# Kernel tuning notes

Measured on AMD Instinct MI355X. Metric: run time of the kernel, lower is better.

The kernel has to match this reference:

```python
import jax, jax.numpy as jnp
import numpy as np

B, T, C = 4, 2048, 1024
H, D = 16, 64  # num_heads, head_size


def setup_inputs() -> dict:
    key = jax.random.key(0)
    ks = jax.random.split(key, 5)
    s = 0.02
    x = jax.random.normal(ks[0], (B, T, C), dtype=jnp.float32)
    Wq = jax.random.normal(ks[1], (H, C, D), dtype=jnp.float32) * s
    Wk = jax.random.normal(ks[2], (H, C, D), dtype=jnp.float32) * s
    Wv = jax.random.normal(ks[3], (H, C, D), dtype=jnp.float32) * s
    Wp = jax.random.normal(ks[4], (C, H * D), dtype=jnp.float32) * s  # Linear(H*D, C) weight
    bp = jnp.zeros((C,), dtype=jnp.float32)
    return {"x": x, "Wq": Wq, "Wk": Wk, "Wv": Wv, "Wp": Wp, "bp": bp}


def reference(x, Wq, Wk, Wv, Wp, bp):
    # per-head projections (all heads batched): [B,T,C] x [H,C,D] -> [B,H,T,D]
    q = jnp.einsum('btc,hcd->bhtd', x, Wq)
    k = jnp.einsum('btc,hcd->bhtd', x, Wk)
    v = jnp.einsum('btc,hcd->bhtd', x, Wv)
    scale = 1.0 / jnp.sqrt(jnp.asarray(D, dtype=x.dtype))
    scores = jnp.einsum('bhtd,bhsd->bhts', q, k) * scale  # [B,H,T,T]
    causal = jnp.tril(jnp.ones((T, T), dtype=bool))
    scores = jnp.where(causal, scores, -jnp.inf)
    w = jax.nn.softmax(scores, axis=-1)
    out = jnp.einsum('bhts,bhsd->bhtd', w, v)  # [B,H,T,D]
    out = out.transpose(0, 2, 1, 3).reshape(B, T, H * D)  # concat heads
    return out @ Wp.T + bp  # projection (dropout is identity in eval)
```

## Files before the change

### kernel.cpp

```cpp
#include <hip/hip_runtime.h>
#include <stdint.h>


typedef unsigned short u16;
typedef __attribute__((ext_vector_type(8))) short    s16x8;
typedef __attribute__((ext_vector_type(4))) float    f32x4;
typedef __attribute__((ext_vector_type(2))) uint32_t u32x2;


__device__ __forceinline__ u16 f2b(float f) {
  union { float f; uint32_t u; } v; v.f = f;
  uint32_t r = v.u + 0x7FFFu + ((v.u >> 16) & 1u);
  return (u16)(r >> 16);
}

__device__ __forceinline__ uint32_t cvtpk(float a, float b) {
  uint32_t r;
  asm("v_cvt_pk_bf16_f32 %0, %1, %2" : "=v"(r) : "v"(a), "v"(b));
  return r;
}

__device__ __forceinline__ f32x4 mfma_bf16(s16x8 a, s16x8 b, f32x4 c) {
  asm("v_mfma_f32_16x16x32_bf16 %0, %1, %2, %0" : "+v"(c) : "v"(a), "v"(b));
  return c;
}

__device__ __forceinline__ void gload_lds16(const void* g, void* l) {
  __builtin_amdgcn_global_load_lds(
      (__attribute__((address_space(1))) void*)(uintptr_t)g,
      (__attribute__((address_space(3))) void*)(uint32_t)(uintptr_t)l,
      16, 0, 0);
}


__global__ void cvt_all_kernel(const float* __restrict__ x, const float* __restrict__ Wq,
                               const float* __restrict__ Wk, const float* __restrict__ Wv,
                               const float* __restrict__ Wp, u16* __restrict__ xb,
                               u16* __restrict__ wqkvb, u16* __restrict__ wpb) {
  int bid = blockIdx.x;
  if (bid < 4608) {
    const float* src = (bid < 4096) ? x : Wp;
    u16* dst = (bid < 4096) ? xb : wpb;
    size_t i = (size_t)((bid < 4096) ? bid : (bid - 4096)) * 256 + threadIdx.x;
    const f32x4* pp = (const f32x4*)(src + i * 8);
    f32x4 a = pp[0], b2 = pp[1];
    s16x8 o;
    o[0]=(short)f2b(a[0]); o[1]=(short)f2b(a[1]); o[2]=(short)f2b(a[2]); o[3]=(short)f2b(a[3]);
    o[4]=(short)f2b(b2[0]); o[5]=(short)f2b(b2[1]); o[6]=(short)f2b(b2[2]); o[7]=(short)f2b(b2[3]);
    *(s16x8*)(dst + i * 8) = o;
  } else {
    int idx = (bid - 4608) * 256 + threadIdx.x;
    int sel = idx >> 20;
    int rem = idx & 1048575;
    int n = rem >> 10, c = rem & 1023;
    int h = n >> 6, d = n & 63;
    const float* W = (sel == 0) ? Wq : ((sel == 1) ? Wk : Wv);
    wqkvb[idx] = f2b(W[h * 65536 + c * 64 + d]);
  }
}


template <int MODE>
__global__ __launch_bounds__(256) void gemm_bt_kernel(
    const u16* __restrict__ A, const u16* __restrict__ B, void* __restrict__ Cout,
    const float* __restrict__ bias, u16* __restrict__ vTout, int K, int ldc)
{
  __shared__ __attribute__((aligned(16))) u16 As[128 * 64];
  __shared__ __attribute__((aligned(16))) u16 Bs[128 * 64];

  const int tid  = threadIdx.x;
  const int lane = tid & 63;
  const int w    = tid >> 6;
  const int wm   = w >> 1, wn = w & 1;
  const int g    = lane >> 4;
  const int li   = lane & 15;

  const int nbx = gridDim.x;
  const int nb  = nbx * gridDim.y;
  const int bid = blockIdx.x + nbx * blockIdx.y;
  const int chunk = nb >> 3;
  const int bid2 = (bid & 7) * chunk + (bid >> 3);
  const size_t bm = (size_t)(bid2 % nbx) * 128;
  const size_t bn = (size_t)(bid2 / nbx) * 128;

  f32x4 acc[4][4] = {};

  const int kIters = K >> 6;
  for (int kt = 0; kt < kIters; ++kt) {
    const int kb = kt * 64;
#pragma unroll
    for (int i = 0; i < 4; ++i) {
      int c = i * 256 + tid;
      int row = c >> 3, sl = c & 7;
      int ss = sl ^ (row & 7);
      gload_lds16(A + (bm + row) * K + kb + ss * 8, &As[c * 8]);
      gload_lds16(B + (bn + row) * K + kb + ss * 8, &Bs[c * 8]);
    }
    __syncthreads();
#pragma unroll
    for (int ks = 0; ks < 2; ++ks) {
      s16x8 af[4], bfr[4];
#pragma unroll
      for (int f = 0; f < 4; ++f) {
        int ra = wm * 64 + f * 16 + li;
        int sa = (ks * 4 + g) ^ (ra & 7);
        af[f] = *(const s16x8*)&As[ra * 64 + sa * 8];
        int rb = wn * 64 + f * 16 + li;
        int sb = (ks * 4 + g) ^ (rb & 7);
        bfr[f] = *(const s16x8*)&Bs[rb * 64 + sb * 8];
      }
#pragma unroll
      for (int mi = 0; mi < 4; ++mi)
#pragma unroll
        for (int ni = 0; ni < 4; ++ni)
          acc[mi][ni] = mfma_bf16(af[mi], bfr[ni], acc[mi][ni]);
    }
    __syncthreads();
  }

  if constexpr (MODE == 1) {
#pragma unroll
    for (int ni = 0; ni < 4; ++ni) {
      size_t col = bn + wn * 64 + ni * 16 + li;
      float bv = bias[col];
#pragma unroll
      for (int mi = 0; mi < 4; ++mi)
#pragma unroll
        for (int r = 0; r < 4; ++r) {
          size_t row = bm + wm * 64 + mi * 16 + g * 4 + r;
          ((float*)Cout)[row * ldc + col] = acc[mi][ni][r] + bv;
        }
    }
  } else {
    if (bn < 2048) {
#pragma unroll
      for (int ni = 0; ni < 4; ++ni) {
        size_t col = bn + wn * 64 + ni * 16 + li;
#pragma unroll
        for (int mi = 0; mi < 4; ++mi)
#pragma unroll
          for (int r = 0; r < 4; ++r) {
            size_t row = bm + wm * 64 + mi * 16 + g * 4 + r;
            ((u16*)Cout)[row * ldc + col] = f2b(acc[mi][ni][r]);
          }
      }
    } else {
      const int hb = (int)((bn - 2048) >> 6) + wn;
      const int bb = (int)(bm >> 11);
      const int t0b = ((int)bm & 2047) + wm * 64 + g * 4;
      u16* vrow = vTout + (size_t)((bb * 16 + hb) * 64) * 2048;
#pragma unroll
      for (int ni = 0; ni < 4; ++ni) {
        u16* vd_ = vrow + (size_t)(ni * 16 + li) * 2048;
#pragma unroll
        for (int mi = 0; mi < 4; ++mi) {
          u32x2 wv = { cvtpk(acc[mi][ni][0], acc[mi][ni][1]),
                       cvtpk(acc[mi][ni][2], acc[mi][ni][3]) };
          *(u32x2*)&vd_[t0b + mi * 16] = wv;
        }
      }
    }
  }
}


__global__ __launch_bounds__(256, 4) void attn_kernel(const u16* __restrict__ qkv,
                                                      const u16* __restrict__ vT,
                                                      u16* __restrict__ out) {
  __shared__ __attribute__((aligned(16))) u16 Ks[2][64 * 64];
  __shared__ __attribute__((aligned(16))) u16 Vs[2][64 * 64];
  __shared__ __attribute__((aligned(16))) u16 Ps[4][16 * 64];

  const int id  = blockIdx.x;
  const int xcd = id & 7;
  const int rr  = id >> 3;
  const int bh  = xcd * 8 + (rr & 7);
  const int p   = rr >> 3;

  const int b = bh >> 4, h = bh & 15;
  const int tid = threadIdx.x;
  const int lane = tid & 63;
  const int w = tid >> 6;
  const int g = lane >> 4, li = lane & 15;

  const int tA = 31 - p;
  const int nA = tA + 1;
  const int nTot = 33;

  const u16* kbase = qkv + (size_t)(b * 2048) * 3072 + 1024 + h * 64;
  const u16* vtb   = vT + (size_t)bh * 64 * 2048;
  u16* pl = Ps[w];

  const int srow = tid >> 3;
  const int ssl0 = (tid & 7) ^ (srow & 7);
  const int kge0 = srow * 3072 + ssl0 * 8;
  const int vge0 = srow * 2048 + ssl0 * 8;
  u16* const kd0 = &Ks[0][tid * 8];
  u16* const vd0 = &Vs[0][tid * 8];

  int foff[2][4];
#pragma unroll
  for (int kk = 0; kk < 2; ++kk)
#pragma unroll
    for (int fj = 0; fj < 4; ++fj) {
      int rk = fj * 16 + li;
      foff[kk][fj] = rk * 64 + (((kk * 4 + g) ^ (rk & 7)) * 8);
    }
  const int lsw = li & 14;
  int pwoff[4], proff[2];
#pragma unroll
  for (int fj = 0; fj < 4; ++fj) pwoff[fj] = li * 64 + (((4 * fj + g) ^ lsw) * 4);
#pragma unroll
  for (int kk = 0; kk < 2; ++kk) proff[kk] = li * 64 + (((8 * kk + 2 * g) ^ lsw) * 4);

  auto stage = [&](int buf, int j0) {
    const u16* kp = kbase + (size_t)j0 * 3072;
    const u16* vp = vtb + j0;
    u16* kd = kd0 + buf * 4096;
    u16* vd = vd0 + buf * 4096;
    gload_lds16(kp + kge0, kd);
    gload_lds16(kp + kge0 + 32 * 3072, kd + 2048);
    gload_lds16(vp + vge0, vd);
    gload_lds16(vp + vge0 + 32 * 2048, vd + 2048);
  };

  stage(0, 0);
  __syncthreads();

  s16x8 qf[2];
  f32x4 oacc[4];
  float mrow = -1e30f, lrowp = 0.f;
  int qglob = 0;
  const float cexp = 0.18033688011112042f;
  const float thr = 8.0f;

  for (int s = 0; s < nTot; ++s) {
    const int cur = s & 1;
    const bool inA = s < nA;
    const int t  = inA ? s : s - nA;
    const int qt = inA ? tA : p;
    const int j0 = t * 64;

    if (s + 1 < nTot) {
      int t1 = (s + 1 < nA) ? (s + 1) : (s + 1 - nA);
      stage(cur ^ 1, t1 * 64);
    }

    if (t == 0) {
      qglob = qt * 64 + w * 16 + li;
      const u16* qbase = qkv + (size_t)(b * 2048 + qglob) * 3072 + h * 64;
#pragma unroll
      for (int kk = 0; kk < 2; ++kk)
        qf[kk] = *(const s16x8*)&qbase[kk * 32 + g * 8];
      mrow = -1e30f; lrowp = 0.f;
#pragma unroll
      for (int fd = 0; fd < 4; ++fd) oacc[fd] = (f32x4)0.f;
    }

    const u16* ksb = &Ks[0][0] + cur * 4096;
    const u16* vsb = &Vs[0][0] + cur * 4096;

    f32x4 sfr[4] = {};
    __builtin_amdgcn_s_setprio(1);
#pragma unroll
    for (int kk = 0; kk < 2; ++kk) {
      s16x8 kf[4];
#pragma unroll
      for (int fj = 0; fj < 4; ++fj) kf[fj] = *(const s16x8*)&ksb[foff[kk][fj]];
#pragma unroll
      for (int fj = 0; fj < 4; ++fj) sfr[fj] = mfma_bf16(kf[fj], qf[kk], sfr[fj]);
    }
    __builtin_amdgcn_s_setprio(0);

    if (t == qt) {
#pragma unroll
      for (int fj = 0; fj < 4; ++fj)
#pragma unroll
        for (int r = 0; r < 4; ++r) {
          int jj = j0 + fj * 16 + g * 4 + r;
          if (jj > qglob) sfr[fj][r] = -1e30f;
        }
    }

    float mx = sfr[0][0];
#pragma unroll
    for (int fj = 0; fj < 4; ++fj)
#pragma unroll
      for (int r = 0; r < 4; ++r) mx = fmaxf(mx, sfr[fj][r]);

    bool need = (mx - mrow) * cexp > thr;
    if (__any(need)) {
      float m0 = mx;
      m0 = fmaxf(m0, __shfl_xor(m0, 16));
      m0 = fmaxf(m0, __shfl_xor(m0, 32));
      float mnew = fmaxf(mrow, m0);
      float sc = exp2f((mrow - mnew) * cexp);
      mrow = mnew;
      lrowp *= sc;
#pragma unroll
      for (int fd = 0; fd < 4; ++fd)
#pragma unroll
        for (int r = 0; r < 4; ++r) oacc[fd][r] *= sc;
    }

    float rs = 0.f;
#pragma unroll
    for (int fj = 0; fj < 4; ++fj) {
      float p0 = exp2f((sfr[fj][0] - mrow) * cexp);
      float p1 = exp2f((sfr[fj][1] - mrow) * cexp);
      float p2 = exp2f((sfr[fj][2] - mrow) * cexp);
      float p3 = exp2f((sfr[fj][3] - mrow) * cexp);
      rs += (p0 + p1) + (p2 + p3);
      u32x2 wv = { cvtpk(p0, p1), cvtpk(p2, p3) };
      *(u32x2*)&pl[pwoff[fj]] = wv;
    }
    lrowp += rs;

    __builtin_amdgcn_s_setprio(1);
#pragma unroll
    for (int kk = 0; kk < 2; ++kk) {
      s16x8 pf = *(const s16x8*)&pl[proff[kk]];
      s16x8 vf[4];
#pragma unroll
      for (int fd = 0; fd < 4; ++fd) vf[fd] = *(const s16x8*)&vsb[foff[kk][fd]];
#pragma unroll
      for (int fd = 0; fd < 4; ++fd) oacc[fd] = mfma_bf16(vf[fd], pf, oacc[fd]);
    }
    __builtin_amdgcn_s_setprio(0);

    if (t == qt) {
      float lr = lrowp;
      lr += __shfl_xor(lr, 16);
      lr += __shfl_xor(lr, 32);
      float inv = 1.f / lr;
      u16* ob = out + (size_t)(b * 2048 + qglob) * 1024 + h * 64;
#pragma unroll
      for (int fd = 0; fd < 4; ++fd) {
        u32x2 wv = { cvtpk(oacc[fd][0] * inv, oacc[fd][1] * inv),
                     cvtpk(oacc[fd][2] * inv, oacc[fd][3] * inv) };
        *(u32x2*)&ob[fd * 16 + g * 4] = wv;
      }
    }

    __syncthreads();
  }
}


extern "C" void kernel_launch(void* const* d_in, const int* in_sizes, int n_in,
                              void* d_out, int out_size, void* d_ws, size_t ws_size,
                              hipStream_t stream) {
  const float* x  = (const float*)d_in[0];
  const float* Wq = (const float*)d_in[1];
  const float* Wk = (const float*)d_in[2];
  const float* Wv = (const float*)d_in[3];
  const float* Wp = (const float*)d_in[4];
  const float* bp = (const float*)d_in[5];
  (void)in_sizes; (void)n_in; (void)out_size; (void)ws_size;

  char* ws = (char*)d_ws;
  u16* xb    = (u16*)(ws);
  u16* wqkvb = (u16*)(ws + 16777216);
  u16* wpb   = (u16*)(ws + 23068672);
  u16* qkv   = (u16*)(ws + 25165824);
  u16* vT    = (u16*)(ws + 75497472);
  u16* ao    = (u16*)(ws + 92274688);

  cvt_all_kernel<<<16896, 256, 0, stream>>>(x, Wq, Wk, Wv, Wp, xb, wqkvb, wpb);

  gemm_bt_kernel<2><<<dim3(64, 24), 256, 0, stream>>>(
      xb, wqkvb, (void*)qkv, nullptr, vT, 1024, 3072);

  attn_kernel<<<1024, 256, 0, stream>>>(qkv, vT, ao);

  gemm_bt_kernel<1><<<dim3(64, 8), 256, 0, stream>>>(
      ao, wpb, d_out, bp, nullptr, 1024, 1024);
}
```

Before: 184.7 us.

## Use 128-wide KV tiles in attention and drop GEMM block swizzle

The attention kernel now processes 128 keys per iteration instead of 64. That halves the number of loop iterations and __syncthreads barriers, at the cost of doubling LDS per block and lowering the launch-bounds occupancy target from 4 to 2 blocks. The P and V LDS layouts and swizzle offsets are reworked for the wider tile, and causal masking moves to the last tile of each query block. Separately, the GEMM drops its XCD-aware block-index remapping and uses plain blockIdx tiling, which may change L2 locality.

```diff
diff --git a/kernel.cpp b/kernel.cpp
--- a/kernel.cpp
+++ b/kernel.cpp
@@ -74,14 +74,8 @@
   const int wm   = w >> 1, wn = w & 1;
   const int g    = lane >> 4;
   const int li   = lane & 15;
-
-  const int nbx = gridDim.x;
-  const int nb  = nbx * gridDim.y;
-  const int bid = blockIdx.x + nbx * blockIdx.y;
-  const int chunk = nb >> 3;
-  const int bid2 = (bid & 7) * chunk + (bid >> 3);
-  const size_t bm = (size_t)(bid2 % nbx) * 128;
-  const size_t bn = (size_t)(bid2 / nbx) * 128;
+  const size_t bm = (size_t)blockIdx.x * 128;
+  const size_t bn = (size_t)blockIdx.y * 128;
 
   f32x4 acc[4][4] = {};
 
@@ -164,12 +158,12 @@
 }
 
 
-__global__ __launch_bounds__(256, 4) void attn_kernel(const u16* __restrict__ qkv,
+__global__ __launch_bounds__(256, 2) void attn_kernel(const u16* __restrict__ qkv,
                                                       const u16* __restrict__ vT,
                                                       u16* __restrict__ out) {
-  __shared__ __attribute__((aligned(16))) u16 Ks[2][64 * 64];
-  __shared__ __attribute__((aligned(16))) u16 Vs[2][64 * 64];
-  __shared__ __attribute__((aligned(16))) u16 Ps[4][16 * 64];
+  __shared__ __attribute__((aligned(16))) u16 Ks[2][128 * 64];
+  __shared__ __attribute__((aligned(16))) u16 Vs[2][64 * 128];
+  __shared__ __attribute__((aligned(16))) u16 Ps[4][16 * 128];
 
   const int id  = blockIdx.x;
   const int xcd = id & 7;
@@ -183,45 +177,53 @@
   const int w = tid >> 6;
   const int g = lane >> 4, li = lane & 15;
 
-  const int tA = 31 - p;
-  const int nA = tA + 1;
-  const int nTot = 33;
+  const int nA = ((31 - p) >> 1) + 1;
+  const int nB = (p >> 1) + 1;
+  const int nTot = 17;
 
   const u16* kbase = qkv + (size_t)(b * 2048) * 3072 + 1024 + h * 64;
   const u16* vtb   = vT + (size_t)bh * 64 * 2048;
   u16* pl = Ps[w];
 
-  const int srow = tid >> 3;
-  const int ssl0 = (tid & 7) ^ (srow & 7);
-  const int kge0 = srow * 3072 + ssl0 * 8;
-  const int vge0 = srow * 2048 + ssl0 * 8;
+  const int kge0 = (tid >> 3) * 3072 + (((tid & 7) ^ ((tid >> 3) & 7)) * 8);
+  const int vge0 = (tid >> 4) * 2048 + (((tid & 15) ^ ((tid >> 4) & 7)) * 8);
   u16* const kd0 = &Ks[0][tid * 8];
   u16* const vd0 = &Vs[0][tid * 8];
 
-  int foff[2][4];
+  int foffK[2][8];
 #pragma unroll
   for (int kk = 0; kk < 2; ++kk)
 #pragma unroll
-    for (int fj = 0; fj < 4; ++fj) {
+    for (int fj = 0; fj < 8; ++fj) {
       int rk = fj * 16 + li;
-      foff[kk][fj] = rk * 64 + (((kk * 4 + g) ^ (rk & 7)) * 8);
-    }
-  const int lsw = li & 14;
-  int pwoff[4], proff[2];
-#pragma unroll
-  for (int fj = 0; fj < 4; ++fj) pwoff[fj] = li * 64 + (((4 * fj + g) ^ lsw) * 4);
-#pragma unroll
-  for (int kk = 0; kk < 2; ++kk) proff[kk] = li * 64 + (((8 * kk + 2 * g) ^ lsw) * 4);
+      foffK[kk][fj] = rk * 64 + (((kk * 4 + g) ^ (rk & 7)) * 8);
+    }
+  int foffV[4][4];
+#pragma unroll
+  for (int cc = 0; cc < 4; ++cc)
+#pragma unroll
+    for (int fd = 0; fd < 4; ++fd) {
+      int rv = fd * 16 + li;
+      foffV[cc][fd] = rv * 128 + (((cc * 4 + g) ^ (rv & 7)) * 8);
+    }
+  int pwoff[8], proff[4];
+#pragma unroll
+  for (int fj = 0; fj < 8; ++fj)
+    pwoff[fj] = li * 128 + (((fj * 2 + (g >> 1)) ^ (li & 15)) * 8) + (g & 1) * 4;
+#pragma unroll
+  for (int cc = 0; cc < 4; ++cc)
+    proff[cc] = li * 128 + (((cc * 4 + g) ^ (li & 15)) * 8);
 
   auto stage = [&](int buf, int j0) {
-    const u16* kp = kbase + (size_t)j0 * 3072;
-    const u16* vp = vtb + j0;
-    u16* kd = kd0 + buf * 4096;
-    u16* vd = vd0 + buf * 4096;
-    gload_lds16(kp + kge0, kd);
-    gload_lds16(kp + kge0 + 32 * 3072, kd + 2048);
-    gload_lds16(vp + vge0, vd);
-    gload_lds16(vp + vge0 + 32 * 2048, vd + 2048);
+    const u16* kp = kbase + (size_t)j0 * 3072 + kge0;
+    const u16* vp = vtb + j0 + vge0;
+    u16* kd = kd0 + buf * 8192;
+    u16* vd = vd0 + buf * 8192;
+#pragma unroll
+    for (int i = 0; i < 4; ++i) {
+      gload_lds16(kp + i * 98304, kd + i * 2048);
+      gload_lds16(vp + i * 32768, vd + i * 2048);
+    }
   };
 
   stage(0, 0);
@@ -238,12 +240,13 @@
     const int cur = s & 1;
     const bool inA = s < nA;
     const int t  = inA ? s : s - nA;
-    const int qt = inA ? tA : p;
-    const int j0 = t * 64;
+    const int qt = inA ? (31 - p) : p;
+    const int nq = inA ? nA : nB;
+    const int j0 = t * 128;
 
     if (s + 1 < nTot) {
       int t1 = (s + 1 < nA) ? (s + 1) : (s + 1 - nA);
-      stage(cur ^ 1, t1 * 64);
+      stage(cur ^ 1, t1 * 128);
     }
 
     if (t == 0) {
@@ -257,24 +260,26 @@
       for (int fd = 0; fd < 4; ++fd) oacc[fd] = (f32x4)0.f;
     }
 
-    const u16* ksb = &Ks[0][0] + cur * 4096;
-    const u16* vsb = &Vs[0][0] + cur * 4096;
-
-    f32x4 sfr[4] = {};
+    const u16* ksb = &Ks[0][0] + cur * 8192;
+    const u16* vsb = &Vs[0][0] + cur * 8192;
+
+    f32x4 sfr[8];
+#pragma unroll
+    for (int fj = 0; fj < 8; ++fj) sfr[fj] = (f32x4)0.f;
     __builtin_amdgcn_s_setprio(1);
 #pragma unroll
     for (int kk = 0; kk < 2; ++kk) {
-      s16x8 kf[4];
-#pragma unroll
-      for (int fj = 0; fj < 4; ++fj) kf[fj] = *(const s16x8*)&ksb[foff[kk][fj]];
-#pragma unroll
-      for (int fj = 0; fj < 4; ++fj) sfr[fj] = mfma_bf16(kf[fj], qf[kk], sfr[fj]);
+      s16x8 kf[8];
+#pragma unroll
+      for (int fj = 0; fj < 8; ++fj) kf[fj] = *(const s16x8*)&ksb[foffK[kk][fj]];
+#pragma unroll
+      for (int fj = 0; fj < 8; ++fj) sfr[fj] = mfma_bf16(kf[fj], qf[kk], sfr[fj]);
     }
     __builtin_amdgcn_s_setprio(0);
 
-    if (t == qt) {
-#pragma unroll
-      for (int fj = 0; fj < 4; ++fj)
+    if (t == nq - 1) {
+#pragma unroll
+      for (int fj = 0; fj < 8; ++fj)
 #pragma unroll
         for (int r = 0; r < 4; ++r) {
           int jj = j0 + fj * 16 + g * 4 + r;
@@ -284,7 +289,7 @@
 
     float mx = sfr[0][0];
 #pragma unroll
-    for (int fj = 0; fj < 4; ++fj)
+    for (int fj = 0; fj < 8; ++fj)
 #pragma unroll
       for (int r = 0; r < 4; ++r) mx = fmaxf(mx, sfr[fj][r]);
 
@@ -305,7 +310,7 @@
 
     float rs = 0.f;
 #pragma unroll
-    for (int fj = 0; fj < 4; ++fj) {
+    for (int fj = 0; fj < 8; ++fj) {
       float p0 = exp2f((sfr[fj][0] - mrow) * cexp);
       float p1 = exp2f((sfr[fj][1] - mrow) * cexp);
       float p2 = exp2f((sfr[fj][2] - mrow) * cexp);
@@ -318,17 +323,17 @@
 
     __builtin_amdgcn_s_setprio(1);
 #pragma unroll
-    for (int kk = 0; kk < 2; ++kk) {
-      s16x8 pf = *(const s16x8*)&pl[proff[kk]];
+    for (int cc = 0; cc < 4; ++cc) {
+      s16x8 pf = *(const s16x8*)&pl[proff[cc]];
       s16x8 vf[4];
 #pragma unroll
-      for (int fd = 0; fd < 4; ++fd) vf[fd] = *(const s16x8*)&vsb[foff[kk][fd]];
+      for (int fd = 0; fd < 4; ++fd) vf[fd] = *(const s16x8*)&vsb[foffV[cc][fd]];
 #pragma unroll
       for (int fd = 0; fd < 4; ++fd) oacc[fd] = mfma_bf16(vf[fd], pf, oacc[fd]);
     }
     __builtin_amdgcn_s_setprio(0);
 
-    if (t == qt) {
+    if (t == nq - 1) {
       float lr = lrowp;
       lr += __shfl_xor(lr, 16);
       lr += __shfl_xor(lr, 32);
```

Result: faster. 174.6 us (-5.4%).
